# Optimization experiments

Hardware: AMD Instinct MI355X
Metric: run time of the kernel (lower is better)

## Reference

```python
import jax, jax.numpy as jnp
import numpy as np

EMBED = 384
N_HEADS = 6
HEAD_SIZE = EMBED // N_HEADS
B, T = 4, 2048
EPS = 1e-5


def _layernorm(x, g, b):
    mu = jnp.mean(x, axis=-1, keepdims=True)
    var = jnp.mean(jnp.square(x - mu), axis=-1, keepdims=True)
    return (x - mu) * jax.lax.rsqrt(var + EPS) * g + b


def setup_inputs() -> dict:
    key = jax.random.key(0)
    ks = jax.random.split(key, 6)
    s = 0.02
    return {
        "x": jax.random.normal(ks[0], (B, T, EMBED), jnp.float32),
        "Wq": jax.random.normal(ks[1], (N_HEADS, HEAD_SIZE, EMBED), jnp.float32) * s,
        "Wo": jax.random.normal(ks[2], (EMBED, EMBED), jnp.float32) * s,
        "bo": jnp.zeros((EMBED,), jnp.float32),
        "W1": jax.random.normal(ks[3], (EMBED, EMBED), jnp.float32) * s,
        "b1": jnp.zeros((EMBED,), jnp.float32),
        "W2": jax.random.normal(ks[4], (EMBED, EMBED), jnp.float32) * s,
        "b2": jnp.zeros((EMBED,), jnp.float32),
        "g1": jnp.ones((EMBED,), jnp.float32),
        "be1": jnp.zeros((EMBED,), jnp.float32),
        "g2": jnp.ones((EMBED,), jnp.float32),
        "be2": jnp.zeros((EMBED,), jnp.float32),
    }


def reference(x, Wq, Wo, bo, W1, b1, W2, b2, g1, be1, g2, be2):
    # NOTE: original Head uses self.query for q, k AND v (a bug we reproduce):
    # q = k = v = x @ Wq^T per head.
    q = jnp.einsum("bte,hde->bhtd", x, Wq)  # [B,H,T,D]
    scale = HEAD_SIZE ** -0.5
    scores = jnp.einsum("bhtd,bhsd->bhts", q, q) * scale  # [B,H,T,T]
    # torch.tril zeros the upper triangle, then masked_fill(tmp==0, -inf)
    tril = jnp.tril(jnp.ones((T, T), bool))
    scores = jnp.where(tril, scores, 0.0)
    scores = jnp.where(scores == 0.0, -jnp.inf, scores)
    attn = jax.nn.softmax(scores, axis=-1)
    head_out = jnp.einsum("bhts,bhsd->bhtd", attn, q)  # [B,H,T,D]
    cat = head_out.transpose(0, 2, 1, 3).reshape(B, T, EMBED)  # concat heads
    sa = cat @ Wo.T + bo
    x = _layernorm(x + sa, g1, be1)
    ff = jax.nn.relu(x @ W1.T + b1) @ W2.T + b2
    return _layernorm(x + ff, g2, be2)
```

## Files before the change

### kernel.cpp

```cpp
#include <hip/hip_runtime.h>
#include <math.h>

#define BB 4
#define TT 2048
#define EE 384
#define HH 6
#define DD 64
#define MM (BB*TT)

typedef __attribute__((ext_vector_type(8))) short bf16x8;
typedef __attribute__((ext_vector_type(4))) float f32x4;

__device__ __forceinline__ unsigned short f2bf(float f) {
    unsigned int u = __float_as_uint(f);
    u = (u + 0x7FFFu + ((u >> 16) & 1u)) >> 16;
    return (unsigned short)u;
}
__device__ __forceinline__ float bf2f(unsigned short u) {
    return __uint_as_float(((unsigned int)u) << 16);
}
__device__ __forceinline__ unsigned int pk2(float a, float b) {
    return (unsigned int)f2bf(a) | ((unsigned int)f2bf(b) << 16);
}

__global__ __launch_bounds__(256) void k_cvt(const float* __restrict__ wq,
                                             const float* __restrict__ wo,
                                             const float* __restrict__ w1,
                                             const float* __restrict__ w2,
                                             unsigned short* __restrict__ wqb,
                                             unsigned short* __restrict__ wob,
                                             unsigned short* __restrict__ w1b,
                                             unsigned short* __restrict__ w2b)
{
    int wi = blockIdx.x / 144, off = (blockIdx.x % 144) * 256;
    const float* s4[4] = {wq, wo, w1, w2};
    unsigned short* d4[4] = {wqb, wob, w1b, w2b};
    const float* src = s4[wi]; unsigned short* dst = d4[wi];
    int i = off + threadIdx.x;
    float4 v = ((const float4*)src)[i];
    uint2 o; o.x = pk2(v.x, v.y); o.y = pk2(v.z, v.w);
    ((uint2*)dst)[i] = o;
}

__global__ __launch_bounds__(256, 2) void k_qgemm(const float* __restrict__ x,
                                                  const unsigned short* __restrict__ W,
                                                  unsigned short* __restrict__ qbf,
                                                  unsigned short* __restrict__ qbfT)
{
    __shared__ unsigned short Xs[32][396];
    __shared__ unsigned short Ts[32][200];
    const int tid = threadIdx.x;
    const int w = tid >> 6, lane = tid & 63;
    const int fr = lane & 15, quad = lane >> 4;
    const int m0 = blockIdx.x * 32;
    const int n0 = blockIdx.y * 192 + w * 48;
    const unsigned short* Wp = W + (size_t)(n0 + fr) * EE + quad * 8;

    {
        const float* xp = x + (size_t)m0 * EE;
        #pragma unroll
        for (int it = 0; it < 12; it++) {
            int idx = it * 1024 + tid * 4;
            int row = idx / EE, col = idx % EE;
            float4 v = *(const float4*)(xp + idx);
            uint2 o; o.x = pk2(v.x, v.y); o.y = pk2(v.z, v.w);
            *(uint2*)&Xs[row][col] = o;
        }
    }

    f32x4 acc[2][3];
    bf16x8 bc[3], bn[3];
    #pragma unroll
    for (int mt = 0; mt < 2; mt++)
        #pragma unroll
        for (int nt = 0; nt < 3; nt++) acc[mt][nt] = (f32x4){0.f, 0.f, 0.f, 0.f};
    #pragma unroll
    for (int nt = 0; nt < 3; nt++) bc[nt] = *(const bf16x8*)(Wp + (size_t)nt * 16 * EE);
    __syncthreads();

    #pragma unroll
    for (int k0 = 0; k0 < 12; k0++) {
        if (k0 < 11) {
            #pragma unroll
            for (int nt = 0; nt < 3; nt++)
                bn[nt] = *(const bf16x8*)(Wp + (size_t)nt * 16 * EE + (k0 + 1) * 32);
        }
        bf16x8 a0 = *(const bf16x8*)&Xs[fr][k0 * 32 + quad * 8];
        bf16x8 a1 = *(const bf16x8*)&Xs[16 + fr][k0 * 32 + quad * 8];
        #pragma unroll
        for (int nt = 0; nt < 3; nt++) {
            acc[0][nt] = __builtin_amdgcn_mfma_f32_16x16x32_bf16(a0, bc[nt], acc[0][nt], 0, 0, 0);
            acc[1][nt] = __builtin_amdgcn_mfma_f32_16x16x32_bf16(a1, bc[nt], acc[1][nt], 0, 0, 0);
        }
        #pragma unroll
        for (int nt = 0; nt < 3; nt++) bc[nt] = bn[nt];
    }

    const int bglob = m0 >> 11, t0 = m0 & 2047;
    #pragma unroll
    for (int nt = 0; nt < 3; nt++) {
        int nl = w * 48 + nt * 16 + fr;
        int n = blockIdx.y * 192 + nl;
        int h = n >> 6, d = n & 63;
        #pragma unroll
        for (int mt = 0; mt < 2; mt++)
            #pragma unroll
            for (int r = 0; r < 4; r++) {
                int ml = mt * 16 + quad * 4 + r;
                unsigned short bf = f2bf(acc[mt][nt][r]);
                qbf[((size_t)(bglob * HH + h) * TT + t0 + ml) * DD + d] = bf;
                Ts[ml][nl] = bf;
            }
    }
    __syncthreads();
    if (tid < 192) {
        int nl = tid;
        int n = blockIdx.y * 192 + nl;
        int h = n >> 6, d = n & 63;
        unsigned short tmp[32];
        #pragma unroll
        for (int i = 0; i < 32; i++) tmp[i] = Ts[i][nl];
        unsigned short* dst = qbfT + ((size_t)(bglob * HH + h) * DD + d) * TT + t0;
        *(uint4*)(dst)      = *(const uint4*)&tmp[0];
        *(uint4*)(dst + 8)  = *(const uint4*)&tmp[8];
        *(uint4*)(dst + 16) = *(const uint4*)&tmp[16];
        *(uint4*)(dst + 24) = *(const uint4*)&tmp[24];
    }
}

__global__ __launch_bounds__(256, 4) void k_attn(const unsigned short* __restrict__ qbf,
                                                 const unsigned short* __restrict__ qbfT,
                                                 unsigned short* __restrict__ cat)
{
    __shared__ unsigned short Qs[32][72];
    __shared__ unsigned short Ks[2][64][72];
    __shared__ unsigned short Vs[2][64][72];
    __shared__ unsigned short Ps[32][72];
    __shared__ float lsc[32];
    float (*Oc)[68] = (float(*)[68])&Ks[0][0][0];

    const int id = blockIdx.x;
    const int xcd = id & 7, j = id >> 3;
    const int bh = xcd * 3 + (j % 3);
    const int p = j / 3;
    const int bb = bh / HH, hh = bh % HH;
    const int tid = threadIdx.x;
    const int w = tid >> 6, lane = tid & 63;
    const int qhalf = w & 1, keyhalf = w >> 1;
    const int fr = lane & 15, quad = lane >> 4;
    const int fc = quad * 8;
    const unsigned short* qb  = qbf  + (size_t)bh * TT * DD;
    const unsigned short* qtb = qbfT + (size_t)bh * DD * TT;
    const int lr = tid >> 2, lc = (tid & 3) * 16;
    const int qr = tid >> 3, qc = (tid & 7) * 8;

    #pragma unroll 1
    for (int ph = 0; ph < 2; ph++) {
        const int tile = ph ? (63 - p) : p;
        const int m0 = tile * 32;
        const int nkt = (tile >> 1) + 1;

        uint4 kr0, kr1, vr0, vr1;
        {
            const unsigned short* kp = qb + (size_t)lr * DD + lc;
            kr0 = *(const uint4*)(kp);
            kr1 = *(const uint4*)(kp + 8);
            const unsigned short* vp = qtb + (size_t)lr * TT + lc;
            vr0 = *(const uint4*)(vp);
            vr1 = *(const uint4*)(vp + 8);
        }

        __syncthreads();
        {
            const unsigned short* qp = qb + (size_t)(m0 + qr) * DD + qc;
            *(uint4*)&Qs[qr][qc] = *(const uint4*)(qp);
        }
        *(uint4*)&Ks[0][lr][lc]     = kr0;
        *(uint4*)&Ks[0][lr][lc + 8] = kr1;
        *(uint4*)&Vs[0][lr][lc]     = vr0;
        *(uint4*)&Vs[0][lr][lc + 8] = vr1;
        __syncthreads();
        const bf16x8 qA0 = *(const bf16x8*)&Qs[qhalf * 16 + fr][fc];
        const bf16x8 qA1 = *(const bf16x8*)&Qs[qhalf * 16 + fr][fc + 32];

        f32x4 accO[4];
        #pragma unroll
        for (int dt = 0; dt < 4; dt++) accO[dt] = (f32x4){0.f, 0.f, 0.f, 0.f};
        float ls[4] = {0.f, 0.f, 0.f, 0.f};
        const int rowbase = m0 + qhalf * 16 + quad * 4;
        const int prow = qhalf * 16 + quad * 4;

        for (int kt = 0; kt < nkt; kt++) {
            const int cur = kt & 1;
            const int s0 = kt * 64;
            if (kt < nkt - 1) {
                const unsigned short* kp = qb + (size_t)(s0 + 64 + lr) * DD + lc;
                kr0 = *(const uint4*)(kp);
                kr1 = *(const uint4*)(kp + 8);
                const unsigned short* vp = qtb + (size_t)lr * TT + s0 + 64 + lc;
                vr0 = *(const uint4*)(vp);
                vr1 = *(const uint4*)(vp + 8);
            }

            f32x4 S[2];
            #pragma unroll
            for (int nt = 0; nt < 2; nt++) {
                f32x4 acc = (f32x4){0.f, 0.f, 0.f, 0.f};
                bf16x8 b0 = *(const bf16x8*)&Ks[cur][keyhalf * 32 + nt * 16 + fr][fc];
                acc = __builtin_amdgcn_mfma_f32_16x16x32_bf16(qA0, b0, acc, 0, 0, 0);
                bf16x8 b1 = *(const bf16x8*)&Ks[cur][keyhalf * 32 + nt * 16 + fr][fc + 32];
                acc = __builtin_amdgcn_mfma_f32_16x16x32_bf16(qA1, b1, acc, 0, 0, 0);
                S[nt] = acc;
            }

            #pragma unroll
            for (int nt = 0; nt < 2; nt++) {
                int jg = s0 + keyhalf * 32 + nt * 16 + fr;
                #pragma unroll
                for (int r = 0; r < 4; r++) {
                    float v = S[nt][r] * 0.125f;
                    float pv = (jg <= rowbase + r && v != 0.0f) ? __expf(v) : 0.0f;
                    ls[r] += pv;
                    Ps[prow + r][keyhalf * 32 + nt * 16 + fr] = f2bf(pv);
                }
            }

            bf16x8 pA = *(const bf16x8*)&Ps[qhalf * 16 + fr][keyhalf * 32 + fc];
            #pragma unroll
            for (int dt = 0; dt < 4; dt++) {
                bf16x8 v0 = *(const bf16x8*)&Vs[cur][dt * 16 + fr][keyhalf * 32 + fc];
                accO[dt] = __builtin_amdgcn_mfma_f32_16x16x32_bf16(pA, v0, accO[dt], 0, 0, 0);
            }

            if (kt < nkt - 1) {
                *(uint4*)&Ks[cur ^ 1][lr][lc]     = kr0;
                *(uint4*)&Ks[cur ^ 1][lr][lc + 8] = kr1;
                *(uint4*)&Vs[cur ^ 1][lr][lc]     = vr0;
                *(uint4*)&Vs[cur ^ 1][lr][lc + 8] = vr1;
                __syncthreads();
            }
        }

        __syncthreads();
        #pragma unroll
        for (int r = 0; r < 4; r++) {
            #pragma unroll
            for (int o = 1; o < 16; o <<= 1) ls[r] += __shfl_xor(ls[r], o, 64);
        }
        if (keyhalf == 1) {
            #pragma unroll
            for (int dt = 0; dt < 4; dt++)
                #pragma unroll
                for (int r = 0; r < 4; r++)
                    Oc[prow + r][dt * 16 + fr] = accO[dt][r];
            if (fr == 0) {
                #pragma unroll
                for (int r = 0; r < 4; r++) lsc[prow + r] = ls[r];
            }
        }
        __syncthreads();
        if (keyhalf == 0) {
            float lt[4];
            #pragma unroll
            for (int r = 0; r < 4; r++) lt[r] = ls[r] + lsc[prow + r];
            #pragma unroll
            for (int dt = 0; dt < 4; dt++) {
                #pragma unroll
                for (int r = 0; r < 4; r++) {
                    float o = accO[dt][r] + Oc[prow + r][dt * 16 + fr];
                    int t = rowbase + r;
                    cat[((size_t)bb * TT + t) * EE + hh * DD + dt * 16 + fr] =
                        f2bf(o / lt[r]);
                }
            }
        }
    }
}

__global__ __launch_bounds__(512, 2) void k_ffn(const unsigned short* __restrict__ catb,
                                                const unsigned short* __restrict__ wob,
                                                const float* __restrict__ bo,
                                                const float* __restrict__ x,
                                                const float* __restrict__ g1,
                                                const float* __restrict__ be1,
                                                const unsigned short* __restrict__ w1b,
                                                const float* __restrict__ b1,
                                                const unsigned short* __restrict__ w2b,
                                                const float* __restrict__ b2,
                                                const float* __restrict__ g2,
                                                const float* __restrict__ be2,
                                                float* __restrict__ out)
{
    __shared__ unsigned short X1s[32][392];
    __shared__ unsigned short H1s[32][392];
    __shared__ float ssum[32][8];
    __shared__ float ssq[32][8];
    const int tid = threadIdx.x;
    const int w = tid >> 6, lane = tid & 63;
    const int fr = lane & 15, quad = lane >> 4;
    const int m0 = blockIdx.x * 32;
    const int n0 = w * 48;

    f32x4 acc[2][3];
    bf16x8 bc[3], bn[3];
    const unsigned short* Wp1 = w1b + (size_t)(n0 + fr) * EE + quad * 8;
    const unsigned short* Wp2 = w2b + (size_t)(n0 + fr) * EE + quad * 8;

    {
        const unsigned short* Ap0 = catb + (size_t)(m0 + fr) * EE + quad * 8;
        const unsigned short* Ap1 = Ap0 + 16 * EE;
        const unsigned short* Wp = wob + (size_t)(n0 + fr) * EE + quad * 8;
        #pragma unroll
        for (int mt = 0; mt < 2; mt++)
            #pragma unroll
            for (int nt = 0; nt < 3; nt++) acc[mt][nt] = (f32x4){0.f, 0.f, 0.f, 0.f};
        #pragma unroll
        for (int nt = 0; nt < 3; nt++) bc[nt] = *(const bf16x8*)(Wp + (size_t)nt * 16 * EE);
        #pragma unroll
        for (int k0 = 0; k0 < 12; k0++) {
            if (k0 < 11) {
                #pragma unroll
                for (int nt = 0; nt < 3; nt++)
                    bn[nt] = *(const bf16x8*)(Wp + (size_t)nt * 16 * EE + (k0 + 1) * 32);
            }
            bf16x8 a0 = *(const bf16x8*)(Ap0 + k0 * 32);
            bf16x8 a1 = *(const bf16x8*)(Ap1 + k0 * 32);
            #pragma unroll
            for (int nt = 0; nt < 3; nt++) {
                acc[0][nt] = __builtin_amdgcn_mfma_f32_16x16x32_bf16(a0, bc[nt], acc[0][nt], 0, 0, 0);
                acc[1][nt] = __builtin_amdgcn_mfma_f32_16x16x32_bf16(a1, bc[nt], acc[1][nt], 0, 0, 0);
            }
            #pragma unroll
            for (int nt = 0; nt < 3; nt++) bc[nt] = bn[nt];
        }
    }
    #pragma unroll
    for (int nt = 0; nt < 3; nt++) bc[nt] = *(const bf16x8*)(Wp1 + (size_t)nt * 16 * EE);
    {
        float s1[2][4] = {{0.f,0.f,0.f,0.f},{0.f,0.f,0.f,0.f}};
        float s2[2][4] = {{0.f,0.f,0.f,0.f},{0.f,0.f,0.f,0.f}};
        #pragma unroll
        for (int nt = 0; nt < 3; nt++) {
            int n = n0 + nt * 16 + fr;
            float bv = bo[n];
            #pragma unroll
            for (int mt = 0; mt < 2; mt++)
                #pragma unroll
                for (int r = 0; r < 4; r++) {
                    float v = acc[mt][nt][r] + bv
                            + x[(size_t)(m0 + mt * 16 + quad * 4 + r) * EE + n];
                    acc[mt][nt][r] = v;
                    s1[mt][r] += v;
                    s2[mt][r] += v * v;
                }
        }
        #pragma unroll
        for (int mt = 0; mt < 2; mt++)
            #pragma unroll
            for (int r = 0; r < 4; r++) {
                #pragma unroll
                for (int o = 1; o < 16; o <<= 1) {
                    s1[mt][r] += __shfl_xor(s1[mt][r], o, 64);
                    s2[mt][r] += __shfl_xor(s2[mt][r], o, 64);
                }
            }
        if (fr == 0) {
            #pragma unroll
            for (int mt = 0; mt < 2; mt++)
                #pragma unroll
                for (int r = 0; r < 4; r++) {
                    ssum[mt * 16 + quad * 4 + r][w] = s1[mt][r];
                    ssq [mt * 16 + quad * 4 + r][w] = s2[mt][r];
                }
        }
    }
    __syncthreads();
    {
        #pragma unroll
        for (int mt = 0; mt < 2; mt++) {
            float mu[4], rs[4];
            #pragma unroll
            for (int r = 0; r < 4; r++) {
                int row = mt * 16 + quad * 4 + r;
                float t1 = 0.f, t2 = 0.f;
                #pragma unroll
                for (int q = 0; q < 8; q++) { t1 += ssum[row][q]; t2 += ssq[row][q]; }
                mu[r] = t1 * (1.0f / EE);
                float var = t2 * (1.0f / EE) - mu[r] * mu[r];
                rs[r] = rsqrtf(var + 1e-5f);
            }
            #pragma unroll
            for (int nt = 0; nt < 3; nt++) {
                int n = n0 + nt * 16 + fr;
                float gv = g1[n], bev = be1[n];
                #pragma unroll
                for (int r = 0; r < 4; r++) {
                    float v = (acc[mt][nt][r] - mu[r]) * rs[r] * gv + bev;
                    X1s[mt * 16 + quad * 4 + r][n] = f2bf(v);
                }
            }
        }
    }
    __syncthreads();

    {
        #pragma unroll
        for (int mt = 0; mt < 2; mt++)
            #pragma unroll
            for (int nt = 0; nt < 3; nt++) acc[mt][nt] = (f32x4){0.f, 0.f, 0.f, 0.f};
        #pragma unroll
        for (int k0 = 0; k0 < 12; k0++) {
            if (k0 < 11) {
                #pragma unroll
                for (int nt = 0; nt < 3; nt++)
                    bn[nt] = *(const bf16x8*)(Wp1 + (size_t)nt * 16 * EE + (k0 + 1) * 32);
            }
            bf16x8 a0 = *(const bf16x8*)&X1s[fr][k0 * 32 + quad * 8];
            bf16x8 a1 = *(const bf16x8*)&X1s[16 + fr][k0 * 32 + quad * 8];
            #pragma unroll
            for (int nt = 0; nt < 3; nt++) {
                acc[0][nt] = __builtin_amdgcn_mfma_f32_16x16x32_bf16(a0, bc[nt], acc[0][nt], 0, 0, 0);
                acc[1][nt] = __builtin_amdgcn_mfma_f32_16x16x32_bf16(a1, bc[nt], acc[1][nt], 0, 0, 0);
            }
            #pragma unroll
            for (int nt = 0; nt < 3; nt++) bc[nt] = bn[nt];
        }
        #pragma unroll
        for (int nt = 0; nt < 3; nt++) bc[nt] = *(const bf16x8*)(Wp2 + (size_t)nt * 16 * EE);
        #pragma unroll
        for (int nt = 0; nt < 3; nt++) {
            int n = n0 + nt * 16 + fr;
            float bv = b1[n];
            #pragma unroll
            for (int mt = 0; mt < 2; mt++)
                #pragma unroll
                for (int r = 0; r < 4; r++)
                    H1s[mt * 16 + quad * 4 + r][n] = f2bf(fmaxf(acc[mt][nt][r] + bv, 0.0f));
        }
    }
    __syncthreads();

    {
        #pragma unroll
        for (int mt = 0; mt < 2; mt++)
            #pragma unroll
            for (int nt = 0; nt < 3; nt++) acc[mt][nt] = (f32x4){0.f, 0.f, 0.f, 0.f};
        #pragma unroll
        for (int k0 = 0; k0 < 12; k0++) {
            if (k0 < 11) {
                #pragma unroll
                for (int nt = 0; nt < 3; nt++)
                    bn[nt] = *(const bf16x8*)(Wp2 + (size_t)nt * 16 * EE + (k0 + 1) * 32);
            }
            bf16x8 a0 = *(const bf16x8*)&H1s[fr][k0 * 32 + quad * 8];
            bf16x8 a1 = *(const bf16x8*)&H1s[16 + fr][k0 * 32 + quad * 8];
            #pragma unroll
            for (int nt = 0; nt < 3; nt++) {
                acc[0][nt] = __builtin_amdgcn_mfma_f32_16x16x32_bf16(a0, bc[nt], acc[0][nt], 0, 0, 0);
                acc[1][nt] = __builtin_amdgcn_mfma_f32_16x16x32_bf16(a1, bc[nt], acc[1][nt], 0, 0, 0);
            }
            #pragma unroll
            for (int nt = 0; nt < 3; nt++) bc[nt] = bn[nt];
        }
    }
    {
        float s1[2][4] = {{0.f,0.f,0.f,0.f},{0.f,0.f,0.f,0.f}};
        float s2[2][4] = {{0.f,0.f,0.f,0.f},{0.f,0.f,0.f,0.f}};
        #pragma unroll
        for (int nt = 0; nt < 3; nt++) {
            int n = n0 + nt * 16 + fr;
            float bv = b2[n];
            #pragma unroll
            for (int mt = 0; mt < 2; mt++)
                #pragma unroll
                for (int r = 0; r < 4; r++) {
                    float v = acc[mt][nt][r] + bv + bf2f(X1s[mt * 16 + quad * 4 + r][n]);
                    acc[mt][nt][r] = v;
                    s1[mt][r] += v;
                    s2[mt][r] += v * v;
                }
        }
        #pragma unroll
        for (int mt = 0; mt < 2; mt++)
            #pragma unroll
            for (int r = 0; r < 4; r++) {
                #pragma unroll
                for (int o = 1; o < 16; o <<= 1) {
                    s1[mt][r] += __shfl_xor(s1[mt][r], o, 64);
                    s2[mt][r] += __shfl_xor(s2[mt][r], o, 64);
                }
            }
        if (fr == 0) {
            #pragma unroll
            for (int mt = 0; mt < 2; mt++)
                #pragma unroll
                for (int r = 0; r < 4; r++) {
                    ssum[mt * 16 + quad * 4 + r][w] = s1[mt][r];
                    ssq [mt * 16 + quad * 4 + r][w] = s2[mt][r];
                }
        }
    }
    __syncthreads();
    {
        #pragma unroll
        for (int mt = 0; mt < 2; mt++) {
            float mu[4], rs[4];
            #pragma unroll
            for (int r = 0; r < 4; r++) {
                int row = mt * 16 + quad * 4 + r;
                float u1 = 0.f, u2 = 0.f;
                #pragma unroll
                for (int q = 0; q < 8; q++) { u1 += ssum[row][q]; u2 += ssq[row][q]; }
                mu[r] = u1 * (1.0f / EE);
                float var = u2 * (1.0f / EE) - mu[r] * mu[r];
                rs[r] = rsqrtf(var + 1e-5f);
            }
            #pragma unroll
            for (int nt = 0; nt < 3; nt++) {
                int n = n0 + nt * 16 + fr;
                float gv = g2[n], bev = be2[n];
                #pragma unroll
                for (int r = 0; r < 4; r++)
                    out[(size_t)(m0 + mt * 16 + quad * 4 + r) * EE + n] =
                        (acc[mt][nt][r] - mu[r]) * rs[r] * gv + bev;
            }
        }
    }
}

extern "C" void kernel_launch(void* const* d_in, const int* in_sizes, int n_in,
                              void* d_out, int out_size, void* d_ws, size_t ws_size,
                              hipStream_t stream) {
    (void)in_sizes; (void)n_in; (void)out_size; (void)ws_size;
    const float* x   = (const float*)d_in[0];
    const float* Wq  = (const float*)d_in[1];
    const float* Wo  = (const float*)d_in[2];
    const float* bo  = (const float*)d_in[3];
    const float* W1  = (const float*)d_in[4];
    const float* b1  = (const float*)d_in[5];
    const float* W2  = (const float*)d_in[6];
    const float* b2  = (const float*)d_in[7];
    const float* g1  = (const float*)d_in[8];
    const float* be1 = (const float*)d_in[9];
    const float* g2  = (const float*)d_in[10];
    const float* be2 = (const float*)d_in[11];
    float* out = (float*)d_out;

    float* ws = (float*)d_ws;
    const size_t SZ = (size_t)MM * EE;
    float* S1 = ws + SZ;
    float* S2 = ws + 2 * SZ;
    float* S3 = ws + 3 * SZ;

    unsigned short* qbf  = (unsigned short*)S1;
    unsigned short* qbfT = qbf + (size_t)BB * HH * TT * DD;
    unsigned short* catb = (unsigned short*)S2;
    unsigned short* wqb  = (unsigned short*)S3;
    unsigned short* wob  = wqb + (size_t)EE * EE;
    unsigned short* w1b  = wob + (size_t)EE * EE;
    unsigned short* w2b  = w1b + (size_t)EE * EE;

    k_cvt<<<dim3(4 * 144), dim3(256), 0, stream>>>(Wq, Wo, W1, W2, wqb, wob, w1b, w2b);
    k_qgemm<<<dim3(MM / 32, 2), dim3(256), 0, stream>>>(x, wqb, qbf, qbfT);
    k_attn<<<dim3(768), dim3(256), 0, stream>>>(qbf, qbfT, catb);
    k_ffn<<<dim3(MM / 32), dim3(512), 0, stream>>>(catb, wob, bo, x, g1, be1,
                                                   w1b, b1, w2b, b2, g2, be2, out);
}
```

Measured before the change: 176.4 us.

## Split attention tile pairs into separate blocks, single-buffer K/V, raise occupancy

The attention kernel no longer pairs a short and a long causal query tile inside one block. It launches 1536 blocks, one query tile each, with the longest tiles scheduled first. K/V shared buffers go from double to single buffering, and P reuses the Q tile's shared memory, which shrinks LDS use so occupancy can rise to 6 blocks per CU. The causal mask is only applied on the diagonal key tile, bf16 packing uses the hardware v_cvt_pk_bf16_f32 instruction, and the final division becomes a reciprocal multiply. Single buffering adds an extra barrier per key tile and exposes load latency, which the higher occupancy is meant to hide.

```diff
diff --git a/kernel.cpp b/kernel.cpp
--- a/kernel.cpp
+++ b/kernel.cpp
@@ -21,6 +21,11 @@
 }
 __device__ __forceinline__ unsigned int pk2(float a, float b) {
     return (unsigned int)f2bf(a) | ((unsigned int)f2bf(b) << 16);
+}
+__device__ __forceinline__ unsigned int cvtpk(float lo, float hi) {
+    unsigned int r;
+    asm("v_cvt_pk_bf16_f32 %0, %1, %2" : "=v"(r) : "v"(lo), "v"(hi));
+    return r;
 }
 
 __global__ __launch_bounds__(256) void k_cvt(const float* __restrict__ wq,
@@ -128,21 +133,21 @@
     }
 }
 
-__global__ __launch_bounds__(256, 4) void k_attn(const unsigned short* __restrict__ qbf,
+__global__ __launch_bounds__(256, 6) void k_attn(const unsigned short* __restrict__ qbf,
                                                  const unsigned short* __restrict__ qbfT,
                                                  unsigned short* __restrict__ cat)
 {
     __shared__ unsigned short Qs[32][72];
-    __shared__ unsigned short Ks[2][64][72];
-    __shared__ unsigned short Vs[2][64][72];
-    __shared__ unsigned short Ps[32][72];
+    __shared__ unsigned short Ks[64][72];
+    __shared__ unsigned short Vs[64][72];
     __shared__ float lsc[32];
-    float (*Oc)[68] = (float(*)[68])&Ks[0][0][0];
+    unsigned short (*Ps)[72] = (unsigned short(*)[72])&Qs[0][0];
+    float (*Oc)[68] = (float(*)[68])&Ks[0][0];
 
     const int id = blockIdx.x;
-    const int xcd = id & 7, j = id >> 3;
-    const int bh = xcd * 3 + (j % 3);
-    const int p = j / 3;
+    const int xcd = id & 7, r3 = id >> 3;
+    const int bh = xcd * 3 + (r3 % 3);
+    const int tile = 63 - (r3 / 3);
     const int bb = bh / HH, hh = bh % HH;
     const int tid = threadIdx.x;
     const int w = tid >> 6, lane = tid & 63;
@@ -154,124 +159,135 @@
     const int lr = tid >> 2, lc = (tid & 3) * 16;
     const int qr = tid >> 3, qc = (tid & 7) * 8;
 
-    #pragma unroll 1
-    for (int ph = 0; ph < 2; ph++) {
-        const int tile = ph ? (63 - p) : p;
-        const int m0 = tile * 32;
-        const int nkt = (tile >> 1) + 1;
-
-        uint4 kr0, kr1, vr0, vr1;
-        {
-            const unsigned short* kp = qb + (size_t)lr * DD + lc;
+    const int m0 = tile * 32;
+    const int nkt = (tile >> 1) + 1;
+
+    {
+        const unsigned short* kp = qb + (size_t)lr * DD + lc;
+        uint4 a0 = *(const uint4*)(kp);
+        uint4 a1 = *(const uint4*)(kp + 8);
+        const unsigned short* vp = qtb + (size_t)lr * TT + lc;
+        uint4 b0 = *(const uint4*)(vp);
+        uint4 b1 = *(const uint4*)(vp + 8);
+        const unsigned short* qp = qb + (size_t)(m0 + qr) * DD + qc;
+        uint4 q0 = *(const uint4*)(qp);
+        *(uint4*)&Ks[lr][lc]     = a0;
+        *(uint4*)&Ks[lr][lc + 8] = a1;
+        *(uint4*)&Vs[lr][lc]     = b0;
+        *(uint4*)&Vs[lr][lc + 8] = b1;
+        *(uint4*)&Qs[qr][qc]     = q0;
+    }
+    __syncthreads();
+    const bf16x8 qA0 = *(const bf16x8*)&Qs[qhalf * 16 + fr][fc];
+    const bf16x8 qA1 = *(const bf16x8*)&Qs[qhalf * 16 + fr][fc + 32];
+    __syncthreads();
+
+    f32x4 accO[4];
+    #pragma unroll
+    for (int dt = 0; dt < 4; dt++) accO[dt] = (f32x4){0.f, 0.f, 0.f, 0.f};
+    float ls[4] = {0.f, 0.f, 0.f, 0.f};
+    const int rowbase = m0 + qhalf * 16 + quad * 4;
+    const int prow = qhalf * 16 + quad * 4;
+
+    uint4 kr0, kr1, vr0, vr1;
+    for (int kt = 0; kt < nkt; kt++) {
+        const int s0 = kt * 64;
+        if (kt < nkt - 1) {
+            const unsigned short* kp = qb + (size_t)(s0 + 64 + lr) * DD + lc;
             kr0 = *(const uint4*)(kp);
             kr1 = *(const uint4*)(kp + 8);
-            const unsigned short* vp = qtb + (size_t)lr * TT + lc;
+            const unsigned short* vp = qtb + (size_t)lr * TT + s0 + 64 + lc;
             vr0 = *(const uint4*)(vp);
             vr1 = *(const uint4*)(vp + 8);
         }
 
-        __syncthreads();
-        {
-            const unsigned short* qp = qb + (size_t)(m0 + qr) * DD + qc;
-            *(uint4*)&Qs[qr][qc] = *(const uint4*)(qp);
-        }
-        *(uint4*)&Ks[0][lr][lc]     = kr0;
-        *(uint4*)&Ks[0][lr][lc + 8] = kr1;
-        *(uint4*)&Vs[0][lr][lc]     = vr0;
-        *(uint4*)&Vs[0][lr][lc + 8] = vr1;
-        __syncthreads();
-        const bf16x8 qA0 = *(const bf16x8*)&Qs[qhalf * 16 + fr][fc];
-        const bf16x8 qA1 = *(const bf16x8*)&Qs[qhalf * 16 + fr][fc + 32];
-
-        f32x4 accO[4];
-        #pragma unroll
-        for (int dt = 0; dt < 4; dt++) accO[dt] = (f32x4){0.f, 0.f, 0.f, 0.f};
-        float ls[4] = {0.f, 0.f, 0.f, 0.f};
-        const int rowbase = m0 + qhalf * 16 + quad * 4;
-        const int prow = qhalf * 16 + quad * 4;
-
-        for (int kt = 0; kt < nkt; kt++) {
-            const int cur = kt & 1;
-            const int s0 = kt * 64;
-            if (kt < nkt - 1) {
-                const unsigned short* kp = qb + (size_t)(s0 + 64 + lr) * DD + lc;
-                kr0 = *(const uint4*)(kp);
-                kr1 = *(const uint4*)(kp + 8);
-                const unsigned short* vp = qtb + (size_t)lr * TT + s0 + 64 + lc;
-                vr0 = *(const uint4*)(vp);
-                vr1 = *(const uint4*)(vp + 8);
-            }
-
-            f32x4 S[2];
-            #pragma unroll
-            for (int nt = 0; nt < 2; nt++) {
-                f32x4 acc = (f32x4){0.f, 0.f, 0.f, 0.f};
-                bf16x8 b0 = *(const bf16x8*)&Ks[cur][keyhalf * 32 + nt * 16 + fr][fc];
-                acc = __builtin_amdgcn_mfma_f32_16x16x32_bf16(qA0, b0, acc, 0, 0, 0);
-                bf16x8 b1 = *(const bf16x8*)&Ks[cur][keyhalf * 32 + nt * 16 + fr][fc + 32];
-                acc = __builtin_amdgcn_mfma_f32_16x16x32_bf16(qA1, b1, acc, 0, 0, 0);
-                S[nt] = acc;
-            }
-
-            #pragma unroll
-            for (int nt = 0; nt < 2; nt++) {
-                int jg = s0 + keyhalf * 32 + nt * 16 + fr;
+        f32x4 S[2];
+        #pragma unroll
+        for (int nt = 0; nt < 2; nt++) {
+            f32x4 acc = (f32x4){0.f, 0.f, 0.f, 0.f};
+            bf16x8 b0 = *(const bf16x8*)&Ks[keyhalf * 32 + nt * 16 + fr][fc];
+            acc = __builtin_amdgcn_mfma_f32_16x16x32_bf16(qA0, b0, acc, 0, 0, 0);
+            bf16x8 b1 = *(const bf16x8*)&Ks[keyhalf * 32 + nt * 16 + fr][fc + 32];
+            acc = __builtin_amdgcn_mfma_f32_16x16x32_bf16(qA1, b1, acc, 0, 0, 0);
+            S[nt] = acc;
+        }
+
+        const bool edge = (kt == nkt - 1);
+        #pragma unroll
+        for (int nt = 0; nt < 2; nt++) {
+            const int col = keyhalf * 32 + nt * 16 + fr;
+            float pv[4];
+            if (edge) {
+                const int jg = s0 + col;
                 #pragma unroll
                 for (int r = 0; r < 4; r++) {
                     float v = S[nt][r] * 0.125f;
-                    float pv = (jg <= rowbase + r && v != 0.0f) ? __expf(v) : 0.0f;
-                    ls[r] += pv;
-                    Ps[prow + r][keyhalf * 32 + nt * 16 + fr] = f2bf(pv);
-                }
-            }
-
-            bf16x8 pA = *(const bf16x8*)&Ps[qhalf * 16 + fr][keyhalf * 32 + fc];
-            #pragma unroll
-            for (int dt = 0; dt < 4; dt++) {
-                bf16x8 v0 = *(const bf16x8*)&Vs[cur][dt * 16 + fr][keyhalf * 32 + fc];
-                accO[dt] = __builtin_amdgcn_mfma_f32_16x16x32_bf16(pA, v0, accO[dt], 0, 0, 0);
-            }
-
-            if (kt < nkt - 1) {
-                *(uint4*)&Ks[cur ^ 1][lr][lc]     = kr0;
-                *(uint4*)&Ks[cur ^ 1][lr][lc + 8] = kr1;
-                *(uint4*)&Vs[cur ^ 1][lr][lc]     = vr0;
-                *(uint4*)&Vs[cur ^ 1][lr][lc + 8] = vr1;
-                __syncthreads();
-            }
-        }
-
-        __syncthreads();
-        #pragma unroll
-        for (int r = 0; r < 4; r++) {
-            #pragma unroll
-            for (int o = 1; o < 16; o <<= 1) ls[r] += __shfl_xor(ls[r], o, 64);
-        }
-        if (keyhalf == 1) {
-            #pragma unroll
-            for (int dt = 0; dt < 4; dt++)
-                #pragma unroll
-                for (int r = 0; r < 4; r++)
-                    Oc[prow + r][dt * 16 + fr] = accO[dt][r];
-            if (fr == 0) {
-                #pragma unroll
-                for (int r = 0; r < 4; r++) lsc[prow + r] = ls[r];
-            }
-        }
-        __syncthreads();
-        if (keyhalf == 0) {
-            float lt[4];
-            #pragma unroll
-            for (int r = 0; r < 4; r++) lt[r] = ls[r] + lsc[prow + r];
-            #pragma unroll
-            for (int dt = 0; dt < 4; dt++) {
-                #pragma unroll
-                for (int r = 0; r < 4; r++) {
-                    float o = accO[dt][r] + Oc[prow + r][dt * 16 + fr];
-                    int t = rowbase + r;
-                    cat[((size_t)bb * TT + t) * EE + hh * DD + dt * 16 + fr] =
-                        f2bf(o / lt[r]);
-                }
+                    pv[r] = (jg <= rowbase + r && v != 0.0f) ? __expf(v) : 0.0f;
+                    ls[r] += pv[r];
+                }
+            } else {
+                #pragma unroll
+                for (int r = 0; r < 4; r++) {
+                    float v = S[nt][r] * 0.125f;
+                    pv[r] = (v != 0.0f) ? __expf(v) : 0.0f;
+                    ls[r] += pv[r];
+                }
+            }
+            unsigned int pk0 = cvtpk(pv[0], pv[1]);
+            unsigned int pk1 = cvtpk(pv[2], pv[3]);
+            Ps[prow + 0][col] = (unsigned short)(pk0);
+            Ps[prow + 1][col] = (unsigned short)(pk0 >> 16);
+            Ps[prow + 2][col] = (unsigned short)(pk1);
+            Ps[prow + 3][col] = (unsigned short)(pk1 >> 16);
+        }
+
+        bf16x8 pA = *(const bf16x8*)&Ps[qhalf * 16 + fr][keyhalf * 32 + fc];
+        #pragma unroll
+        for (int dt = 0; dt < 4; dt++) {
+            bf16x8 v0 = *(const bf16x8*)&Vs[dt * 16 + fr][keyhalf * 32 + fc];
+            accO[dt] = __builtin_amdgcn_mfma_f32_16x16x32_bf16(pA, v0, accO[dt], 0, 0, 0);
+        }
+
+        if (kt < nkt - 1) {
+            __syncthreads();
+            *(uint4*)&Ks[lr][lc]     = kr0;
+            *(uint4*)&Ks[lr][lc + 8] = kr1;
+            *(uint4*)&Vs[lr][lc]     = vr0;
+            *(uint4*)&Vs[lr][lc + 8] = vr1;
+            __syncthreads();
+        }
+    }
+
+    __syncthreads();
+    #pragma unroll
+    for (int r = 0; r < 4; r++) {
+        #pragma unroll
+        for (int o = 1; o < 16; o <<= 1) ls[r] += __shfl_xor(ls[r], o, 64);
+    }
+    if (keyhalf == 1) {
+        #pragma unroll
+        for (int dt = 0; dt < 4; dt++)
+            #pragma unroll
+            for (int r = 0; r < 4; r++)
+                Oc[prow + r][dt * 16 + fr] = accO[dt][r];
+        if (fr == 0) {
+            #pragma unroll
+            for (int r = 0; r < 4; r++) lsc[prow + r] = ls[r];
+        }
+    }
+    __syncthreads();
+    if (keyhalf == 0) {
+        float il[4];
+        #pragma unroll
+        for (int r = 0; r < 4; r++) il[r] = 1.0f / (ls[r] + lsc[prow + r]);
+        #pragma unroll
+        for (int dt = 0; dt < 4; dt++) {
+            #pragma unroll
+            for (int r = 0; r < 4; r++) {
+                float o = accO[dt][r] + Oc[prow + r][dt * 16 + fr];
+                int t = rowbase + r;
+                cat[((size_t)bb * TT + t) * EE + hh * DD + dt * 16 + fr] =
+                    f2bf(o * il[r]);
             }
         }
     }
@@ -562,7 +578,7 @@
 
     k_cvt<<<dim3(4 * 144), dim3(256), 0, stream>>>(Wq, Wo, W1, W2, wqb, wob, w1b, w2b);
     k_qgemm<<<dim3(MM / 32, 2), dim3(256), 0, stream>>>(x, wqb, qbf, qbfT);
-    k_attn<<<dim3(768), dim3(256), 0, stream>>>(qbf, qbfT, catb);
+    k_attn<<<dim3(1536), dim3(256), 0, stream>>>(qbf, qbfT, catb);
     k_ffn<<<dim3(MM / 32), dim3(512), 0, stream>>>(catb, wob, bo, x, g1, be1,
                                                    w1b, b1, w2b, b2, g2, be2, out);
 }
```

Result: slower. 184.7 us (+4.7%).
